# Kernel tuning notes

Measured on AMD Instinct MI355X. Metric: run time of the kernel, lower is better.

Reference implementation:

```python
import jax, jax.numpy as jnp
import numpy as np

B_SZ, SEQ, D_MODEL, D_STATE, DT_RANK = 2, 2048, 1024, 16, 64


def setup_inputs() -> dict:
    key = jax.random.key(0)
    ks = jax.random.split(key, 7)
    x = jax.random.normal(ks[0], (B_SZ, SEQ, D_MODEL), dtype=jnp.float32)
    dt_proj_input = jax.random.normal(ks[1], (B_SZ, SEQ, DT_RANK), dtype=jnp.float32)
    # A_log initialized as -log(arange(1, d_state+1)) per _initialize_parameters
    A_log = -jnp.log(jnp.arange(1, D_STATE + 1, dtype=jnp.float32))
    # dt_proj: weight ~ N(0, 0.1), bias = log(expm1(dt)) - 2 with dt ~ logU(dt_min, dt_max)
    dt_W = 0.1 * jax.random.normal(ks[2], (D_MODEL, DT_RANK), dtype=jnp.float32)
    u = jax.random.uniform(ks[3], (D_MODEL,), dtype=jnp.float32)
    dt = jnp.exp(u * (np.log(0.1) - np.log(0.001)) + np.log(0.001))
    dt = jnp.clip(dt, 0.0001, None)
    dt_b = jnp.log(jnp.expm1(dt)) - 2.0
    # B_proj / C_proj: xavier-uniform (d_state, d_model), no bias
    lim = np.sqrt(6.0 / (D_STATE + D_MODEL)).astype(np.float32)
    B_W = jax.random.uniform(ks[4], (D_STATE, D_MODEL), dtype=jnp.float32, minval=-lim, maxval=lim)
    C_W = jax.random.uniform(ks[5], (D_STATE, D_MODEL), dtype=jnp.float32, minval=-lim, maxval=lim)
    D_vec = jnp.ones((D_MODEL,), dtype=jnp.float32)
    return {"x": x, "dt_proj_input": dt_proj_input, "A_log": A_log,
            "dt_W": dt_W, "dt_b": dt_b, "B_W": B_W, "C_W": C_W, "D_vec": D_vec}


def reference(x, dt_proj_input, A_log, dt_W, dt_b, B_W, C_W, D_vec):
    # dt = softplus(Linear(dt_proj_input) + bias)  -- note bias is added twice, faithful to source
    dt = jax.nn.softplus(jnp.einsum('blr,dr->bld', dt_proj_input, dt_W) + 2.0 * dt_b)  # (b,l,d)
    Bm = jnp.einsum('bld,nd->bln', x, B_W)  # (b,l,n)
    Cm = jnp.einsum('bld,nd->bln', x, C_W)  # (b,l,n)
    A = -jnp.exp(A_log)                      # (n,)
    dA = jnp.exp(dt[..., None] * A)                                   # (b,l,d,n)
    dB = dt[..., None] * Bm[:, :, None, :] * x[..., None]             # (b,l,d,n)
    # linear recurrence h[t] = dA[t] * h[t-1] + dB[t]
    def step(h, ab):
        a, b = ab
        h = a * h + b
        return h, h
    h0 = jnp.zeros((x.shape[0], x.shape[2], A_log.shape[0]), dtype=x.dtype)
    _, states = jax.lax.scan(step, h0, (jnp.swapaxes(dA, 0, 1), jnp.swapaxes(dB, 0, 1)))
    states = jnp.swapaxes(states, 0, 1)      # (b,l,d,n)
    y = jnp.einsum('bldn,bln->bld', states, Cm)
    return y + x * D_vec
```

## Files before the change

kernel.cpp:

```cpp
#include <hip/hip_runtime.h>

#define LOG2E 1.44269504088896340736f
#define LN2   0.69314718055994530942f

constexpr int BSZ = 2, SEQ = 2048, DM = 1024, DS = 16, DR = 64;
constexpr int NC = 64, CL = SEQ / NC;

constexpr size_t OFF_DT   = 0;
constexpr size_t OFF_BM   = OFF_DT + (size_t)BSZ*SEQ*DM;
constexpr size_t OFF_CM   = OFF_BM + (size_t)BSZ*SEQ*DS;
constexpr size_t OFF_S    = OFF_CM + (size_t)BSZ*SEQ*DS;
constexpr size_t OFF_HEND = OFF_S  + (size_t)BSZ*NC*DM;
constexpr size_t OFF_HIN  = OFF_HEND + (size_t)BSZ*NC*DS*DM;
constexpr size_t OFF_PART = OFF_HIN  + (size_t)BSZ*NC*DS*DM;

__device__ inline float softplusf(float z) {
  float e = __builtin_amdgcn_exp2f(z * LOG2E);
  if (z > 15.f) return z;
  if (z < -8.f) return e;
  return __builtin_amdgcn_logf(1.f + e) * LN2;
}

__device__ inline void fma4(float& acc, float4 a, float4 b) {
  acc = fmaf(a.x, b.x, fmaf(a.y, b.y, fmaf(a.z, b.z, fmaf(a.w, b.w, acc))));
}

__global__ __launch_bounds__(256, 2) void k_front(const float* __restrict__ inp,
                                                  const float* __restrict__ W,
                                                  const float* __restrict__ bias,
                                                  float* __restrict__ dt,
                                                  const float* __restrict__ x,
                                                  const float* __restrict__ BW,
                                                  const float* __restrict__ CW,
                                                  float* __restrict__ part) {
  __shared__ __align__(16) float smem[16896];
  int bid = blockIdx.x;
  int t = threadIdx.x;
  if (bid < 256) {
    float* At = smem;
    float* Wt = smem + 64 * 132;
    int mt = bid >> 3, nt = bid & 7;
    int m0 = mt * 128, n0 = nt * 128;
#pragma unroll
    for (int i = 0; i < 8; ++i) {
      int idx4 = t + 256 * i;
      int m = idx4 >> 4, k4 = (idx4 & 15) * 4;
      float4 v = *(const float4*)&inp[(size_t)(m0 + m) * DR + k4];
      At[(k4 + 0) * 132 + m] = v.x; At[(k4 + 1) * 132 + m] = v.y;
      At[(k4 + 2) * 132 + m] = v.z; At[(k4 + 3) * 132 + m] = v.w;
    }
#pragma unroll
    for (int i = 0; i < 8; ++i) {
      int idx4 = t + 256 * i;
      int n = idx4 >> 4, k4 = (idx4 & 15) * 4;
      float4 v = *(const float4*)&W[(size_t)(n0 + n) * DR + k4];
      Wt[(k4 + 0) * 132 + n] = v.x; Wt[(k4 + 1) * 132 + n] = v.y;
      Wt[(k4 + 2) * 132 + n] = v.z; Wt[(k4 + 3) * 132 + n] = v.w;
    }
    __syncthreads();
    int mg = t >> 4, ng = t & 15;
    float acc[8][8] = {};
#pragma unroll 4
    for (int k = 0; k < 64; ++k) {
      const float* rowA = At + k * 132;
      const float* rowW = Wt + k * 132;
      float4 a0 = *(const float4*)&rowA[mg * 8];
      float4 a1 = *(const float4*)&rowA[mg * 8 + 4];
      float4 w0 = *(const float4*)&rowW[ng * 4];
      float4 w1 = *(const float4*)&rowW[ng * 4 + 64];
      float a[8] = {a0.x, a0.y, a0.z, a0.w, a1.x, a1.y, a1.z, a1.w};
      float w[8] = {w0.x, w0.y, w0.z, w0.w, w1.x, w1.y, w1.z, w1.w};
#pragma unroll
      for (int i = 0; i < 8; ++i)
#pragma unroll
        for (int j = 0; j < 8; ++j)
          acc[i][j] = fmaf(a[i], w[j], acc[i][j]);
    }
    float4 b0 = *(const float4*)&bias[n0 + ng * 4];
    float4 b1 = *(const float4*)&bias[n0 + ng * 4 + 64];
    float bb[8] = {b0.x, b0.y, b0.z, b0.w, b1.x, b1.y, b1.z, b1.w};
#pragma unroll
    for (int i = 0; i < 8; ++i) {
      int m = m0 + mg * 8 + i;
      float4 lo, hi;
      lo.x = softplusf(acc[i][0] + 2.f * bb[0]);
      lo.y = softplusf(acc[i][1] + 2.f * bb[1]);
      lo.z = softplusf(acc[i][2] + 2.f * bb[2]);
      lo.w = softplusf(acc[i][3] + 2.f * bb[3]);
      hi.x = softplusf(acc[i][4] + 2.f * bb[4]);
      hi.y = softplusf(acc[i][5] + 2.f * bb[5]);
      hi.z = softplusf(acc[i][6] + 2.f * bb[6]);
      hi.w = softplusf(acc[i][7] + 2.f * bb[7]);
      *(float4*)&dt[(size_t)m * DM + n0 + ng * 4]      = lo;
      *(float4*)&dt[(size_t)m * DM + n0 + ng * 4 + 64] = hi;
    }
  } else {
    float* xt = smem;
    float* wt = smem + 64 * 132;
    int bid2 = bid - 256;
    int mt = bid2 >> 3, ks = bid2 & 7;
    int m0 = mt * 64, k0 = ks * 128;
#pragma unroll
    for (int i = 0; i < 8; ++i) {
      int idx4 = t + 256 * i;
      int r = idx4 >> 5, c4 = (idx4 & 31) * 4;
      float4 v = *(const float4*)&x[(size_t)(m0 + r) * DM + k0 + c4];
      *(float4*)&xt[r * 132 + c4] = v;
    }
#pragma unroll
    for (int i = 0; i < 4; ++i) {
      int idx4 = t + 256 * i;
      int n = idx4 >> 5, c4 = (idx4 & 31) * 4;
      const float* src = (n < 16) ? &BW[(size_t)n * DM + k0 + c4]
                                  : &CW[(size_t)(n - 16) * DM + k0 + c4];
      *(float4*)&wt[n * 132 + c4] = *(const float4*)src;
    }
    __syncthreads();
    int lg = t >> 3, ng = t & 7;
    float acc[2][4] = {};
#pragma unroll 4
    for (int k4 = 0; k4 < 32; ++k4) {
      float4 xa0 = *(const float4*)&xt[(lg * 2 + 0) * 132 + k4 * 4];
      float4 xa1 = *(const float4*)&xt[(lg * 2 + 1) * 132 + k4 * 4];
#pragma unroll
      for (int j = 0; j < 4; ++j) {
        float4 w = *(const float4*)&wt[(ng + 8 * j) * 132 + k4 * 4];
        fma4(acc[0][j], xa0, w);
        fma4(acc[1][j], xa1, w);
      }
    }
#pragma unroll
    for (int i = 0; i < 2; ++i)
#pragma unroll
      for (int j = 0; j < 4; ++j)
        part[(size_t)ks * (4096 * 32) + (size_t)(m0 + lg * 2 + i) * 32 + ng + 8 * j] = acc[i][j];
  }
}

__global__ __launch_bounds__(256) void k_phase1(const float* __restrict__ x,
                                                const float* __restrict__ dt,
                                                const float* __restrict__ part,
                                                const float* __restrict__ A_log,
                                                float* __restrict__ Bm,
                                                float* __restrict__ Cm,
                                                float* __restrict__ Ssum,
                                                float* __restrict__ hend) {
  __shared__ float bml[CL * DS];
  int bid = blockIdx.x;
  int b = bid >> 8, rem = bid & 255;
  int c = rem >> 2, dg = rem & 3;
  int t = threadIdx.x;
  int d = dg * 256 + t;
  size_t blbase = (size_t)b * SEQ + c * CL;
  {
    size_t e = (blbase + (t >> 3)) * 32 + 2 * (t & 7);
    float2 s = make_float2(0.f, 0.f);
#pragma unroll
    for (int ks = 0; ks < 8; ++ks) {
      float2 v = *(const float2*)&part[(size_t)ks * (4096 * 32) + e];
      s.x += v.x; s.y += v.y;
    }
    *(float2*)&bml[t * 2] = s;
    if (dg == 0) {
      *(float2*)&Bm[(blbase + (t >> 3)) * DS + 2 * (t & 7)] = s;
      float2 sc = make_float2(0.f, 0.f);
#pragma unroll
      for (int ks = 0; ks < 8; ++ks) {
        float2 v = *(const float2*)&part[(size_t)ks * (4096 * 32) + e + 16];
        sc.x += v.x; sc.y += v.y;
      }
      *(float2*)&Cm[(blbase + (t >> 3)) * DS + 2 * (t & 7)] = sc;
    }
  }
  __syncthreads();
  float a2[16];
#pragma unroll
  for (int n = 0; n < 16; ++n)
    a2[n] = -__builtin_amdgcn_exp2f(A_log[n] * LOG2E) * LOG2E;
  float h[16] = {};
  float S = 0.f;
  size_t base = blbase * DM + d;
#pragma unroll 4
  for (int l = 0; l < CL; ++l) {
    float dtv = dt[base + (size_t)l * DM];
    float xv  = x[base + (size_t)l * DM];
    S += dtv;
    float dtx = dtv * xv;
#pragma unroll
    for (int n = 0; n < 16; ++n) {
      float a = __builtin_amdgcn_exp2f(dtv * a2[n]);
      h[n] = fmaf(a, h[n], dtx * bml[l * DS + n]);
    }
  }
  size_t cc = (size_t)b * NC + c;
  Ssum[cc * DM + d] = S;
#pragma unroll
  for (int n = 0; n < 16; ++n) hend[(cc * DS + n) * DM + d] = h[n];
}

__global__ __launch_bounds__(256) void k_phase2(const float* __restrict__ A_log,
                                                const float* __restrict__ Ssum,
                                                const float* __restrict__ hend,
                                                float* __restrict__ hin) {
  int bid = blockIdx.x;
  int b = bid >> 6, rem = bid & 63;
  int n = rem >> 2, dg = rem & 3;
  int d = dg * 256 + threadIdx.x;
  float a2 = -__builtin_amdgcn_exp2f(A_log[n] * LOG2E) * LOG2E;
  float h = 0.f;
#pragma unroll 8
  for (int c = 0; c < NC; ++c) {
    size_t cc = (size_t)b * NC + c;
    hin[(cc * DS + n) * DM + d] = h;
    float aa = __builtin_amdgcn_exp2f(a2 * Ssum[cc * DM + d]);
    h = fmaf(aa, h, hend[(cc * DS + n) * DM + d]);
  }
}

__global__ __launch_bounds__(256) void k_phase3(const float* __restrict__ x,
                                                const float* __restrict__ dt,
                                                const float* __restrict__ Bm,
                                                const float* __restrict__ Cm,
                                                const float* __restrict__ A_log,
                                                const float* __restrict__ Dvec,
                                                const float* __restrict__ hin,
                                                float* __restrict__ out) {
  __shared__ float bml[CL * DS], cml[CL * DS];
  int bid = blockIdx.x;
  int b = bid >> 8, rem = bid & 255;
  int c = rem >> 2, dg = rem & 3;
  int t = threadIdx.x;
  int d = dg * 256 + t;
  const float* bsrc = Bm + ((size_t)b * SEQ + c * CL) * DS;
  const float* csrc = Cm + ((size_t)b * SEQ + c * CL) * DS;
  *(float2*)&bml[t * 2] = *(const float2*)&bsrc[t * 2];
  *(float2*)&cml[t * 2] = *(const float2*)&csrc[t * 2];
  __syncthreads();
  float a2[16];
#pragma unroll
  for (int n = 0; n < 16; ++n)
    a2[n] = -__builtin_amdgcn_exp2f(A_log[n] * LOG2E) * LOG2E;
  size_t cc = (size_t)b * NC + c;
  float h[16];
#pragma unroll
  for (int n = 0; n < 16; ++n) h[n] = hin[(cc * DS + n) * DM + d];
  float dv = Dvec[d];
  size_t base = ((size_t)b * SEQ + c * CL) * DM + d;
#pragma unroll 4
  for (int l = 0; l < CL; ++l) {
    float dtv = dt[base + (size_t)l * DM];
    float xv  = x[base + (size_t)l * DM];
    float dtx = dtv * xv;
    float y = 0.f;
#pragma unroll
    for (int n = 0; n < 16; ++n) {
      float a = __builtin_amdgcn_exp2f(dtv * a2[n]);
      h[n] = fmaf(a, h[n], dtx * bml[l * DS + n]);
      y = fmaf(h[n], cml[l * DS + n], y);
    }
    out[base + (size_t)l * DM] = fmaf(xv, dv, y);
  }
}

extern "C" void kernel_launch(void* const* d_in, const int* in_sizes, int n_in,
                              void* d_out, int out_size, void* d_ws, size_t ws_size,
                              hipStream_t stream) {
  (void)in_sizes; (void)n_in; (void)out_size; (void)ws_size;
  const float* x     = (const float*)d_in[0];
  const float* dtp   = (const float*)d_in[1];
  const float* A_log = (const float*)d_in[2];
  const float* dtW   = (const float*)d_in[3];
  const float* dtb   = (const float*)d_in[4];
  const float* BW    = (const float*)d_in[5];
  const float* CW    = (const float*)d_in[6];
  const float* Dv    = (const float*)d_in[7];
  float* out = (float*)d_out;
  float* ws  = (float*)d_ws;

  float* dt   = ws + OFF_DT;
  float* Bm   = ws + OFF_BM;
  float* Cm   = ws + OFF_CM;
  float* S    = ws + OFF_S;
  float* hend = ws + OFF_HEND;
  float* hin  = ws + OFF_HIN;
  float* part = ws + OFF_PART;

  k_front <<<768, 256, 0, stream>>>(dtp, dtW, dtb, dt, x, BW, CW, part);
  k_phase1<<<512, 256, 0, stream>>>(x, dt, part, A_log, Bm, Cm, S, hend);
  k_phase2<<<128, 256, 0, stream>>>(A_log, S, hend, hin);
  k_phase3<<<512, 256, 0, stream>>>(x, dt, Bm, Cm, A_log, Dv, hin, out);
}
```

Before: 64.40 us.

## Split state dimension across lanes and halve K-split partials in front GEMM

The phase1 and phase3 scans now give each channel to two lanes, each handling 8 of the 16 state entries. In phase3 the two halves of y are combined with a cross-lane shuffle. Blocks shrink to 128 threads and the grid grows to 2048 blocks, which raises parallelism and cuts per-thread serial work and register use. The B/C projection in k_front now splits K four ways instead of eight, looping over two K tiles per block, so phase1 reduces fewer partials with float4 loads. In exchange, each lane loads dt and x twice and phase3 adds a shuffle per timestep.

New measurement: 72.14 us. +12.0%, slower.

```diff
diff --git a/kernel.cpp b/kernel.cpp
--- a/kernel.cpp
+++ b/kernel.cpp
@@ -7,10 +7,10 @@
 constexpr int NC = 64, CL = SEQ / NC;
 
 constexpr size_t OFF_DT   = 0;
-constexpr size_t OFF_BM   = OFF_DT + (size_t)BSZ*SEQ*DM;
-constexpr size_t OFF_CM   = OFF_BM + (size_t)BSZ*SEQ*DS;
-constexpr size_t OFF_S    = OFF_CM + (size_t)BSZ*SEQ*DS;
-constexpr size_t OFF_HEND = OFF_S  + (size_t)BSZ*NC*DM;
+constexpr size_t OFF_BM   = OFF_DT   + (size_t)BSZ*SEQ*DM;
+constexpr size_t OFF_CM   = OFF_BM   + (size_t)BSZ*SEQ*DS;
+constexpr size_t OFF_S    = OFF_CM   + (size_t)BSZ*SEQ*DS;
+constexpr size_t OFF_HEND = OFF_S    + (size_t)BSZ*NC*DM;
 constexpr size_t OFF_HIN  = OFF_HEND + (size_t)BSZ*NC*DS*DM;
 constexpr size_t OFF_PART = OFF_HIN  + (size_t)BSZ*NC*DS*DM;
 
@@ -98,35 +98,39 @@
     float* xt = smem;
     float* wt = smem + 64 * 132;
     int bid2 = bid - 256;
-    int mt = bid2 >> 3, ks = bid2 & 7;
-    int m0 = mt * 64, k0 = ks * 128;
-#pragma unroll
-    for (int i = 0; i < 8; ++i) {
-      int idx4 = t + 256 * i;
-      int r = idx4 >> 5, c4 = (idx4 & 31) * 4;
-      float4 v = *(const float4*)&x[(size_t)(m0 + r) * DM + k0 + c4];
-      *(float4*)&xt[r * 132 + c4] = v;
-    }
-#pragma unroll
-    for (int i = 0; i < 4; ++i) {
-      int idx4 = t + 256 * i;
-      int n = idx4 >> 5, c4 = (idx4 & 31) * 4;
-      const float* src = (n < 16) ? &BW[(size_t)n * DM + k0 + c4]
-                                  : &CW[(size_t)(n - 16) * DM + k0 + c4];
-      *(float4*)&wt[n * 132 + c4] = *(const float4*)src;
-    }
-    __syncthreads();
+    int mt = bid2 >> 2, ks = bid2 & 3;
+    int m0 = mt * 64, k0 = ks * 256;
     int lg = t >> 3, ng = t & 7;
     float acc[2][4] = {};
+#pragma unroll
+    for (int kh = 0; kh < 2; ++kh) {
+      int kb = k0 + kh * 128;
+      __syncthreads();
+#pragma unroll
+      for (int i = 0; i < 8; ++i) {
+        int idx4 = t + 256 * i;
+        int r = idx4 >> 5, c4 = (idx4 & 31) * 4;
+        *(float4*)&xt[r * 132 + c4] = *(const float4*)&x[(size_t)(m0 + r) * DM + kb + c4];
+      }
+#pragma unroll
+      for (int i = 0; i < 4; ++i) {
+        int idx4 = t + 256 * i;
+        int n = idx4 >> 5, c4 = (idx4 & 31) * 4;
+        const float* src = (n < 16) ? &BW[(size_t)n * DM + kb + c4]
+                                    : &CW[(size_t)(n - 16) * DM + kb + c4];
+        *(float4*)&wt[n * 132 + c4] = *(const float4*)src;
+      }
+      __syncthreads();
 #pragma unroll 4
-    for (int k4 = 0; k4 < 32; ++k4) {
-      float4 xa0 = *(const float4*)&xt[(lg * 2 + 0) * 132 + k4 * 4];
-      float4 xa1 = *(const float4*)&xt[(lg * 2 + 1) * 132 + k4 * 4];
-#pragma unroll
-      for (int j = 0; j < 4; ++j) {
-        float4 w = *(const float4*)&wt[(ng + 8 * j) * 132 + k4 * 4];
-        fma4(acc[0][j], xa0, w);
-        fma4(acc[1][j], xa1, w);
+      for (int k4 = 0; k4 < 32; ++k4) {
+        float4 xa0 = *(const float4*)&xt[(lg * 2 + 0) * 132 + k4 * 4];
+        float4 xa1 = *(const float4*)&xt[(lg * 2 + 1) * 132 + k4 * 4];
+#pragma unroll
+        for (int j = 0; j < 4; ++j) {
+          float4 w = *(const float4*)&wt[(ng + 8 * j) * 132 + k4 * 4];
+          fma4(acc[0][j], xa0, w);
+          fma4(acc[1][j], xa1, w);
+        }
       }
     }
 #pragma unroll
@@ -137,47 +141,45 @@
   }
 }
 
-__global__ __launch_bounds__(256) void k_phase1(const float* __restrict__ x,
-                                                const float* __restrict__ dt,
-                                                const float* __restrict__ part,
-                                                const float* __restrict__ A_log,
-                                                float* __restrict__ Bm,
-                                                float* __restrict__ Cm,
-                                                float* __restrict__ Ssum,
-                                                float* __restrict__ hend) {
+__global__ __launch_bounds__(128, 4) void k_phase1(const float* __restrict__ x,
+                                                   const float* __restrict__ dt,
+                                                   const float* __restrict__ part,
+                                                   const float* __restrict__ A_log,
+                                                   float* __restrict__ Bm,
+                                                   float* __restrict__ Cm,
+                                                   float* __restrict__ Ssum,
+                                                   float* __restrict__ hend) {
   __shared__ float bml[CL * DS];
   int bid = blockIdx.x;
-  int b = bid >> 8, rem = bid & 255;
-  int c = rem >> 2, dg = rem & 3;
+  int b = bid >> 10, c = (bid >> 4) & 63, dg = bid & 15;
   int t = threadIdx.x;
-  int d = dg * 256 + t;
+  int lane = t & 63, w = t >> 6;
+  int nh = lane >> 5;
+  int d = dg * 64 + (lane & 31) + w * 32;
   size_t blbase = (size_t)b * SEQ + c * CL;
   {
-    size_t e = (blbase + (t >> 3)) * 32 + 2 * (t & 7);
-    float2 s = make_float2(0.f, 0.f);
-#pragma unroll
-    for (int ks = 0; ks < 8; ++ks) {
-      float2 v = *(const float2*)&part[(size_t)ks * (4096 * 32) + e];
-      s.x += v.x; s.y += v.y;
-    }
-    *(float2*)&bml[t * 2] = s;
+    int l = t >> 2, q = (t & 3) * 4;
+    size_t e = (blbase + l) * 32 + q;
+    float4 sb = make_float4(0.f, 0.f, 0.f, 0.f), sc = sb;
+#pragma unroll
+    for (int ks = 0; ks < 4; ++ks) {
+      float4 vb = *(const float4*)&part[(size_t)ks * (4096 * 32) + e];
+      float4 vc = *(const float4*)&part[(size_t)ks * (4096 * 32) + e + 16];
+      sb.x += vb.x; sb.y += vb.y; sb.z += vb.z; sb.w += vb.w;
+      sc.x += vc.x; sc.y += vc.y; sc.z += vc.z; sc.w += vc.w;
+    }
+    *(float4*)&bml[t * 4] = sb;
     if (dg == 0) {
-      *(float2*)&Bm[(blbase + (t >> 3)) * DS + 2 * (t & 7)] = s;
-      float2 sc = make_float2(0.f, 0.f);
-#pragma unroll
-      for (int ks = 0; ks < 8; ++ks) {
-        float2 v = *(const float2*)&part[(size_t)ks * (4096 * 32) + e + 16];
-        sc.x += v.x; sc.y += v.y;
-      }
-      *(float2*)&Cm[(blbase + (t >> 3)) * DS + 2 * (t & 7)] = sc;
+      *(float4*)&Bm[(blbase + l) * DS + q] = sb;
+      *(float4*)&Cm[(blbase + l) * DS + q] = sc;
     }
   }
   __syncthreads();
-  float a2[16];
-#pragma unroll
-  for (int n = 0; n < 16; ++n)
-    a2[n] = -__builtin_amdgcn_exp2f(A_log[n] * LOG2E) * LOG2E;
-  float h[16] = {};
+  float a2[8];
+#pragma unroll
+  for (int j = 0; j < 8; ++j)
+    a2[j] = -__builtin_amdgcn_exp2f(A_log[nh * 8 + j] * LOG2E) * LOG2E;
+  float h[8] = {};
   float S = 0.f;
   size_t base = blbase * DM + d;
 #pragma unroll 4
@@ -186,79 +188,89 @@
     float xv  = x[base + (size_t)l * DM];
     S += dtv;
     float dtx = dtv * xv;
-#pragma unroll
-    for (int n = 0; n < 16; ++n) {
-      float a = __builtin_amdgcn_exp2f(dtv * a2[n]);
-      h[n] = fmaf(a, h[n], dtx * bml[l * DS + n]);
+    const float* bq = &bml[l * DS + nh * 8];
+#pragma unroll
+    for (int j = 0; j < 8; ++j) {
+      float a = __builtin_amdgcn_exp2f(dtv * a2[j]);
+      h[j] = fmaf(a, h[j], dtx * bq[j]);
     }
   }
   size_t cc = (size_t)b * NC + c;
-  Ssum[cc * DM + d] = S;
-#pragma unroll
-  for (int n = 0; n < 16; ++n) hend[(cc * DS + n) * DM + d] = h[n];
-}
-
-__global__ __launch_bounds__(256) void k_phase2(const float* __restrict__ A_log,
-                                                const float* __restrict__ Ssum,
-                                                const float* __restrict__ hend,
-                                                float* __restrict__ hin) {
+  if (nh == 0) Ssum[cc * DM + d] = S;
+#pragma unroll
+  for (int j = 0; j < 8; ++j) hend[(cc * DS + nh * 8 + j) * DM + d] = h[j];
+}
+
+__global__ __launch_bounds__(128, 4) void k_phase2(const float* __restrict__ A_log,
+                                                   const float* __restrict__ Ssum,
+                                                   const float* __restrict__ hend,
+                                                   float* __restrict__ hin) {
   int bid = blockIdx.x;
-  int b = bid >> 6, rem = bid & 63;
-  int n = rem >> 2, dg = rem & 3;
-  int d = dg * 256 + threadIdx.x;
-  float a2 = -__builtin_amdgcn_exp2f(A_log[n] * LOG2E) * LOG2E;
+  int b = bid >> 7, n = (bid >> 3) & 15, dg = bid & 7;
+  int d = dg * 128 + threadIdx.x;
+  float a2n = -__builtin_amdgcn_exp2f(A_log[n] * LOG2E) * LOG2E;
   float h = 0.f;
 #pragma unroll 8
   for (int c = 0; c < NC; ++c) {
     size_t cc = (size_t)b * NC + c;
     hin[(cc * DS + n) * DM + d] = h;
-    float aa = __builtin_amdgcn_exp2f(a2 * Ssum[cc * DM + d]);
+    float aa = __builtin_amdgcn_exp2f(a2n * Ssum[cc * DM + d]);
     h = fmaf(aa, h, hend[(cc * DS + n) * DM + d]);
   }
 }
 
-__global__ __launch_bounds__(256) void k_phase3(const float* __restrict__ x,
-                                                const float* __restrict__ dt,
-                                                const float* __restrict__ Bm,
-                                                const float* __restrict__ Cm,
-                                                const float* __restrict__ A_log,
-                                                const float* __restrict__ Dvec,
-                                                const float* __restrict__ hin,
-                                                float* __restrict__ out) {
+__global__ __launch_bounds__(128, 4) void k_phase3(const float* __restrict__ x,
+                                                   const float* __restrict__ dt,
+                                                   const float* __restrict__ Bm,
+                                                   const float* __restrict__ Cm,
+                                                   const float* __restrict__ A_log,
+                                                   const float* __restrict__ Dvec,
+                                                   const float* __restrict__ hin,
+                                                   float* __restrict__ out) {
   __shared__ float bml[CL * DS], cml[CL * DS];
   int bid = blockIdx.x;
-  int b = bid >> 8, rem = bid & 255;
-  int c = rem >> 2, dg = rem & 3;
+  int b = bid >> 10, c = (bid >> 4) & 63, dg = bid & 15;
   int t = threadIdx.x;
-  int d = dg * 256 + t;
-  const float* bsrc = Bm + ((size_t)b * SEQ + c * CL) * DS;
-  const float* csrc = Cm + ((size_t)b * SEQ + c * CL) * DS;
-  *(float2*)&bml[t * 2] = *(const float2*)&bsrc[t * 2];
-  *(float2*)&cml[t * 2] = *(const float2*)&csrc[t * 2];
+  int lane = t & 63, w = t >> 6;
+  int nh = lane >> 5;
+  int d = dg * 64 + (lane & 31) + w * 32;
+  size_t blbase = (size_t)b * SEQ + c * CL;
+  *(float4*)&bml[t * 4] = *(const float4*)&Bm[blbase * DS + t * 4];
+  *(float4*)&cml[t * 4] = *(const float4*)&Cm[blbase * DS + t * 4];
   __syncthreads();
-  float a2[16];
-#pragma unroll
-  for (int n = 0; n < 16; ++n)
-    a2[n] = -__builtin_amdgcn_exp2f(A_log[n] * LOG2E) * LOG2E;
+  float a2[8];
+#pragma unroll
+  for (int j = 0; j < 8; ++j)
+    a2[j] = -__builtin_amdgcn_exp2f(A_log[nh * 8 + j] * LOG2E) * LOG2E;
   size_t cc = (size_t)b * NC + c;
-  float h[16];
-#pragma unroll
-  for (int n = 0; n < 16; ++n) h[n] = hin[(cc * DS + n) * DM + d];
-  float dv = Dvec[d];
-  size_t base = ((size_t)b * SEQ + c * CL) * DM + d;
+  float h[8];
+#pragma unroll
+  for (int j = 0; j < 8; ++j) h[j] = hin[(cc * DS + nh * 8 + j) * DM + d];
+  float dvl = (nh == 0) ? Dvec[d] : 0.f;
+  size_t base = blbase * DM + d;
 #pragma unroll 4
   for (int l = 0; l < CL; ++l) {
     float dtv = dt[base + (size_t)l * DM];
     float xv  = x[base + (size_t)l * DM];
     float dtx = dtv * xv;
-    float y = 0.f;
-#pragma unroll
-    for (int n = 0; n < 16; ++n) {
-      float a = __builtin_amdgcn_exp2f(dtv * a2[n]);
-      h[n] = fmaf(a, h[n], dtx * bml[l * DS + n]);
-      y = fmaf(h[n], cml[l * DS + n], y);
-    }
-    out[base + (size_t)l * DM] = fmaf(xv, dv, y);
+    const float* bq = &bml[l * DS + nh * 8];
+    const float* cq = &cml[l * DS + nh * 8];
+    float y0 = xv * dvl, y1 = 0.f;
+#pragma unroll
+    for (int j = 0; j < 4; ++j) {
+      float a = __builtin_amdgcn_exp2f(dtv * a2[j]);
+      h[j] = fmaf(a, h[j], dtx * bq[j]);
+      y0 = fmaf(h[j], cq[j], y0);
+    }
+#pragma unroll
+    for (int j = 4; j < 8; ++j) {
+      float a = __builtin_amdgcn_exp2f(dtv * a2[j]);
+      h[j] = fmaf(a, h[j], dtx * bq[j]);
+      y1 = fmaf(h[j], cq[j], y1);
+    }
+    float y = y0 + y1;
+    y += __shfl_xor(y, 32);
+    if (nh == 0) out[base + (size_t)l * DM] = y;
   }
 }
 
@@ -285,8 +297,8 @@
   float* hin  = ws + OFF_HIN;
   float* part = ws + OFF_PART;
 
-  k_front <<<768, 256, 0, stream>>>(dtp, dtW, dtb, dt, x, BW, CW, part);
-  k_phase1<<<512, 256, 0, stream>>>(x, dt, part, A_log, Bm, Cm, S, hend);
-  k_phase2<<<128, 256, 0, stream>>>(A_log, S, hend, hin);
-  k_phase3<<<512, 256, 0, stream>>>(x, dt, Bm, Cm, A_log, Dv, hin, out);
-}
+  k_front <<<512,  256, 0, stream>>>(dtp, dtW, dtb, dt, x, BW, CW, part);
+  k_phase1<<<2048, 128, 0, stream>>>(x, dt, part, A_log, Bm, Cm, S, hend);
+  k_phase2<<<256,  128, 0, stream>>>(A_log, S, hend, hin);
+  k_phase3<<<2048, 128, 0, stream>>>(x, dt, Bm, Cm, A_log, Dv, hin, out);
+}
```

## Fuse chunked scan phases into one cooperative kernel with grid syncs

Applied to the files above, without the earlier changes.

Replaces the three scan kernels with a single cooperative kernel over 1024 blocks and 128 shorter chunks. Each thread keeps its local outputs and cumulative dt in registers, the inter-chunk carry runs between two grid syncs, and the result is corrected with the carried-in state, so dt and x are not re-read in a third pass. The front kernel's B/C projection now splits K four ways instead of eight, halving the partial sums to reduce. The fused path depends on cooperative launch and an occupancy of at least 4 blocks per CU, otherwise it falls back to the old kernels. Large register arrays and a serial carry loop on only 512 blocks of 64 threads risk spills and idle time.

After: 64.76 us. About the same (+0.6%).

```diff
diff --git a/kernel.cpp b/kernel.cpp
--- a/kernel.cpp
+++ b/kernel.cpp
@@ -1,18 +1,22 @@
 #include <hip/hip_runtime.h>
+#include <hip/hip_cooperative_groups.h>
+
+namespace cg = cooperative_groups;
 
 #define LOG2E 1.44269504088896340736f
 #define LN2   0.69314718055994530942f
 
 constexpr int BSZ = 2, SEQ = 2048, DM = 1024, DS = 16, DR = 64;
 constexpr int NC = 64, CL = SEQ / NC;
+constexpr int NCF = 128, CLF = SEQ / NCF;
 
 constexpr size_t OFF_DT   = 0;
-constexpr size_t OFF_BM   = OFF_DT + (size_t)BSZ*SEQ*DM;
-constexpr size_t OFF_CM   = OFF_BM + (size_t)BSZ*SEQ*DS;
-constexpr size_t OFF_S    = OFF_CM + (size_t)BSZ*SEQ*DS;
-constexpr size_t OFF_HEND = OFF_S  + (size_t)BSZ*NC*DM;
-constexpr size_t OFF_HIN  = OFF_HEND + (size_t)BSZ*NC*DS*DM;
-constexpr size_t OFF_PART = OFF_HIN  + (size_t)BSZ*NC*DS*DM;
+constexpr size_t OFF_BM   = OFF_DT   + (size_t)BSZ*SEQ*DM;
+constexpr size_t OFF_CM   = OFF_BM   + (size_t)BSZ*SEQ*DS;
+constexpr size_t OFF_S    = OFF_CM   + (size_t)BSZ*SEQ*DS;
+constexpr size_t OFF_HEND = OFF_S    + (size_t)BSZ*NCF*DM;
+constexpr size_t OFF_HIN  = OFF_HEND + (size_t)BSZ*NCF*DS*DM;
+constexpr size_t OFF_PART = OFF_HIN  + (size_t)BSZ*NCF*DS*DM;
 
 __device__ inline float softplusf(float z) {
   float e = __builtin_amdgcn_exp2f(z * LOG2E);
@@ -98,35 +102,39 @@
     float* xt = smem;
     float* wt = smem + 64 * 132;
     int bid2 = bid - 256;
-    int mt = bid2 >> 3, ks = bid2 & 7;
-    int m0 = mt * 64, k0 = ks * 128;
-#pragma unroll
-    for (int i = 0; i < 8; ++i) {
-      int idx4 = t + 256 * i;
-      int r = idx4 >> 5, c4 = (idx4 & 31) * 4;
-      float4 v = *(const float4*)&x[(size_t)(m0 + r) * DM + k0 + c4];
-      *(float4*)&xt[r * 132 + c4] = v;
-    }
-#pragma unroll
-    for (int i = 0; i < 4; ++i) {
-      int idx4 = t + 256 * i;
-      int n = idx4 >> 5, c4 = (idx4 & 31) * 4;
-      const float* src = (n < 16) ? &BW[(size_t)n * DM + k0 + c4]
-                                  : &CW[(size_t)(n - 16) * DM + k0 + c4];
-      *(float4*)&wt[n * 132 + c4] = *(const float4*)src;
-    }
-    __syncthreads();
+    int mt = bid2 >> 2, ks = bid2 & 3;
+    int m0 = mt * 64, k0 = ks * 256;
     int lg = t >> 3, ng = t & 7;
     float acc[2][4] = {};
+#pragma unroll
+    for (int kh = 0; kh < 2; ++kh) {
+      int kb = k0 + kh * 128;
+      __syncthreads();
+#pragma unroll
+      for (int i = 0; i < 8; ++i) {
+        int idx4 = t + 256 * i;
+        int r = idx4 >> 5, c4 = (idx4 & 31) * 4;
+        *(float4*)&xt[r * 132 + c4] = *(const float4*)&x[(size_t)(m0 + r) * DM + kb + c4];
+      }
+#pragma unroll
+      for (int i = 0; i < 4; ++i) {
+        int idx4 = t + 256 * i;
+        int n = idx4 >> 5, c4 = (idx4 & 31) * 4;
+        const float* src = (n < 16) ? &BW[(size_t)n * DM + kb + c4]
+                                    : &CW[(size_t)(n - 16) * DM + kb + c4];
+        *(float4*)&wt[n * 132 + c4] = *(const float4*)src;
+      }
+      __syncthreads();
 #pragma unroll 4
-    for (int k4 = 0; k4 < 32; ++k4) {
-      float4 xa0 = *(const float4*)&xt[(lg * 2 + 0) * 132 + k4 * 4];
-      float4 xa1 = *(const float4*)&xt[(lg * 2 + 1) * 132 + k4 * 4];
-#pragma unroll
-      for (int j = 0; j < 4; ++j) {
-        float4 w = *(const float4*)&wt[(ng + 8 * j) * 132 + k4 * 4];
-        fma4(acc[0][j], xa0, w);
-        fma4(acc[1][j], xa1, w);
+      for (int k4 = 0; k4 < 32; ++k4) {
+        float4 xa0 = *(const float4*)&xt[(lg * 2 + 0) * 132 + k4 * 4];
+        float4 xa1 = *(const float4*)&xt[(lg * 2 + 1) * 132 + k4 * 4];
+#pragma unroll
+        for (int j = 0; j < 4; ++j) {
+          float4 w = *(const float4*)&wt[(ng + 8 * j) * 132 + k4 * 4];
+          fma4(acc[0][j], xa0, w);
+          fma4(acc[1][j], xa1, w);
+        }
       }
     }
 #pragma unroll
@@ -134,6 +142,106 @@
 #pragma unroll
       for (int j = 0; j < 4; ++j)
         part[(size_t)ks * (4096 * 32) + (size_t)(m0 + lg * 2 + i) * 32 + ng + 8 * j] = acc[i][j];
+  }
+}
+
+__global__ __launch_bounds__(256, 4) void k_scan_fused(const float* __restrict__ x,
+                                                       const float* __restrict__ dtg,
+                                                       const float* __restrict__ part,
+                                                       const float* __restrict__ A_log,
+                                                       const float* __restrict__ Dv,
+                                                       float* __restrict__ Ssum,
+                                                       float* __restrict__ hend,
+                                                       float* __restrict__ hin,
+                                                       float* __restrict__ out) {
+  cg::grid_group grid = cg::this_grid();
+  __shared__ float bml[CLF * DS], cml[CLF * DS];
+  int bid = blockIdx.x, t = threadIdx.x;
+  int b = bid >> 9, c = (bid >> 2) & 127, dg = bid & 3;
+  int d = dg * 256 + t;
+  size_t blbase = (size_t)b * SEQ + (size_t)c * CLF;
+  size_t cc = (size_t)b * NCF + c;
+
+  {
+    int idx = t & 127, l = idx >> 3, pr = idx & 7;
+    int col = pr * 2 + ((t >= 128) ? 16 : 0);
+    size_t e = (blbase + l) * 32 + col;
+    float2 s = make_float2(0.f, 0.f);
+#pragma unroll
+    for (int ks = 0; ks < 4; ++ks) {
+      float2 v = *(const float2*)&part[(size_t)ks * (4096 * 32) + e];
+      s.x += v.x; s.y += v.y;
+    }
+    float* dst = (t < 128) ? bml : cml;
+    *(float2*)&dst[l * DS + pr * 2] = s;
+  }
+  __syncthreads();
+  float a2[16];
+#pragma unroll
+  for (int n = 0; n < 16; ++n)
+    a2[n] = -__builtin_amdgcn_exp2f(A_log[n] * LOG2E) * LOG2E;
+  float Tl[CLF], yl[CLF], h[16] = {};
+  float dv = Dv[d];
+  float T = 0.f;
+  size_t base = blbase * DM + d;
+#pragma unroll
+  for (int l = 0; l < CLF; ++l) {
+    float dtv = dtg[base + (size_t)l * DM];
+    float xv  = x[base + (size_t)l * DM];
+    T += dtv; Tl[l] = T;
+    float dtx = dtv * xv;
+    float y = xv * dv;
+    float bq[16], cq[16];
+#pragma unroll
+    for (int u = 0; u < 4; ++u) {
+      *(float4*)&bq[4 * u] = *(const float4*)&bml[l * DS + 4 * u];
+      *(float4*)&cq[4 * u] = *(const float4*)&cml[l * DS + 4 * u];
+    }
+#pragma unroll
+    for (int n = 0; n < 16; ++n) {
+      float a = __builtin_amdgcn_exp2f(dtv * a2[n]);
+      h[n] = fmaf(a, h[n], dtx * bq[n]);
+      y = fmaf(h[n], cq[n], y);
+    }
+    yl[l] = y;
+  }
+  Ssum[cc * DM + d] = T;
+#pragma unroll
+  for (int n = 0; n < 16; ++n) hend[(cc * DS + n) * DM + d] = h[n];
+
+  grid.sync();
+
+  if (bid < 512 && t < 64) {
+    int b2 = bid >> 8, n = (bid >> 4) & 15, ds16 = bid & 15;
+    int d2 = ds16 * 64 + t;
+    float a2n = -__builtin_amdgcn_exp2f(A_log[n] * LOG2E) * LOG2E;
+    float hh = 0.f;
+#pragma unroll 8
+    for (int c2 = 0; c2 < NCF; ++c2) {
+      size_t cc2 = (size_t)b2 * NCF + c2;
+      hin[(cc2 * DS + n) * DM + d2] = hh;
+      float aa = __builtin_amdgcn_exp2f(a2n * Ssum[cc2 * DM + d2]);
+      hh = fmaf(aa, hh, hend[(cc2 * DS + n) * DM + d2]);
+    }
+  }
+
+  grid.sync();
+
+  float hn[16];
+#pragma unroll
+  for (int n = 0; n < 16; ++n) hn[n] = hin[(cc * DS + n) * DM + d];
+#pragma unroll
+  for (int l = 0; l < CLF; ++l) {
+    float y = yl[l];
+#pragma unroll
+    for (int u = 0; u < 4; ++u) {
+      float4 cq = *(const float4*)&cml[l * DS + 4 * u];
+      y = fmaf(cq.x * hn[4 * u + 0], __builtin_amdgcn_exp2f(a2[4 * u + 0] * Tl[l]), y);
+      y = fmaf(cq.y * hn[4 * u + 1], __builtin_amdgcn_exp2f(a2[4 * u + 1] * Tl[l]), y);
+      y = fmaf(cq.z * hn[4 * u + 2], __builtin_amdgcn_exp2f(a2[4 * u + 2] * Tl[l]), y);
+      y = fmaf(cq.w * hn[4 * u + 3], __builtin_amdgcn_exp2f(a2[4 * u + 3] * Tl[l]), y);
+    }
+    out[base + (size_t)l * DM] = y;
   }
 }
 
@@ -147,28 +255,22 @@
                                                 float* __restrict__ hend) {
   __shared__ float bml[CL * DS];
   int bid = blockIdx.x;
-  int b = bid >> 8, rem = bid & 255;
-  int c = rem >> 2, dg = rem & 3;
+  int b = bid >> 8, c = (bid >> 2) & 63, dg = bid & 3;
   int t = threadIdx.x;
   int d = dg * 256 + t;
   size_t blbase = (size_t)b * SEQ + c * CL;
   {
     size_t e = (blbase + (t >> 3)) * 32 + 2 * (t & 7);
-    float2 s = make_float2(0.f, 0.f);
-#pragma unroll
-    for (int ks = 0; ks < 8; ++ks) {
-      float2 v = *(const float2*)&part[(size_t)ks * (4096 * 32) + e];
-      s.x += v.x; s.y += v.y;
-    }
-    *(float2*)&bml[t * 2] = s;
+    float2 sb = make_float2(0.f, 0.f), sc = make_float2(0.f, 0.f);
+#pragma unroll
+    for (int ks = 0; ks < 4; ++ks) {
+      float2 vb = *(const float2*)&part[(size_t)ks * (4096 * 32) + e];
+      float2 vc = *(const float2*)&part[(size_t)ks * (4096 * 32) + e + 16];
+      sb.x += vb.x; sb.y += vb.y; sc.x += vc.x; sc.y += vc.y;
+    }
+    *(float2*)&bml[t * 2] = sb;
     if (dg == 0) {
-      *(float2*)&Bm[(blbase + (t >> 3)) * DS + 2 * (t & 7)] = s;
-      float2 sc = make_float2(0.f, 0.f);
-#pragma unroll
-      for (int ks = 0; ks < 8; ++ks) {
-        float2 v = *(const float2*)&part[(size_t)ks * (4096 * 32) + e + 16];
-        sc.x += v.x; sc.y += v.y;
-      }
+      *(float2*)&Bm[(blbase + (t >> 3)) * DS + 2 * (t & 7)] = sb;
       *(float2*)&Cm[(blbase + (t >> 3)) * DS + 2 * (t & 7)] = sc;
     }
   }
@@ -203,16 +305,15 @@
                                                 const float* __restrict__ hend,
                                                 float* __restrict__ hin) {
   int bid = blockIdx.x;
-  int b = bid >> 6, rem = bid & 63;
-  int n = rem >> 2, dg = rem & 3;
+  int b = bid >> 6, n = (bid >> 2) & 15, dg = bid & 3;
   int d = dg * 256 + threadIdx.x;
-  float a2 = -__builtin_amdgcn_exp2f(A_log[n] * LOG2E) * LOG2E;
+  float a2n = -__builtin_amdgcn_exp2f(A_log[n] * LOG2E) * LOG2E;
   float h = 0.f;
 #pragma unroll 8
   for (int c = 0; c < NC; ++c) {
     size_t cc = (size_t)b * NC + c;
     hin[(cc * DS + n) * DM + d] = h;
-    float aa = __builtin_amdgcn_exp2f(a2 * Ssum[cc * DM + d]);
+    float aa = __builtin_amdgcn_exp2f(a2n * Ssum[cc * DM + d]);
     h = fmaf(aa, h, hend[(cc * DS + n) * DM + d]);
   }
 }
@@ -227,8 +328,7 @@
                                                 float* __restrict__ out) {
   __shared__ float bml[CL * DS], cml[CL * DS];
   int bid = blockIdx.x;
-  int b = bid >> 8, rem = bid & 255;
-  int c = rem >> 2, dg = rem & 3;
+  int b = bid >> 8, c = (bid >> 2) & 63, dg = bid & 3;
   int t = threadIdx.x;
   int d = dg * 256 + t;
   const float* bsrc = Bm + ((size_t)b * SEQ + c * CL) * DS;
@@ -285,7 +385,21 @@
   float* hin  = ws + OFF_HIN;
   float* part = ws + OFF_PART;
 
-  k_front <<<768, 256, 0, stream>>>(dtp, dtW, dtb, dt, x, BW, CW, part);
+  k_front<<<512, 256, 0, stream>>>(dtp, dtW, dtb, dt, x, BW, CW, part);
+
+  int nb = 0;
+  hipError_t oe = hipOccupancyMaxActiveBlocksPerMultiprocessor(&nb, k_scan_fused, 256, 0);
+  bool coop_ok = (oe == hipSuccess && nb >= 4);
+  if (coop_ok) {
+    const float* xx = x; const float* dd = dt; const float* pp = part;
+    const float* al = A_log; const float* dv = Dv;
+    float* ss = S; float* he = hend; float* hi = hin; float* oo = out;
+    void* kargs[] = {(void*)&xx, (void*)&dd, (void*)&pp, (void*)&al, (void*)&dv,
+                     (void*)&ss, (void*)&he, (void*)&hi, (void*)&oo};
+    hipError_t le = hipLaunchCooperativeKernel((const void*)k_scan_fused,
+                                               dim3(1024), dim3(256), kargs, 0, stream);
+    if (le == hipSuccess) return;
+  }
   k_phase1<<<512, 256, 0, stream>>>(x, dt, part, A_log, Bm, Cm, S, hend);
   k_phase2<<<128, 256, 0, stream>>>(A_log, S, hend, hin);
   k_phase3<<<512, 256, 0, stream>>>(x, dt, Bm, Cm, A_log, Dv, hin, out);
```

## Double scan chunk count, parallelize inter-chunk pass, halve split-K partials

Applied to the files above, without the earlier changes.

Doubles the number of sequence chunks to 128, so the phase-1 and phase-3 scan kernels launch twice as many blocks with half the sequential length each. The inter-chunk carry kernel now splits the 128 chunks into four segments per thread group, computes local prefix states and cumulative dt sums, and combines the segments through shared memory, giving more blocks and shorter serial chains. The B/C projection in the front kernel now uses split-K of 4 with two K-halves per block, which halves the partial-sum traffic read in phase 1. In exchange, the workspace traffic for hend and hin doubles and phase 2 holds 64 extra registers per thread.

Result: slower. 70.72 us (+9.8%).

```diff
diff --git a/kernel.cpp b/kernel.cpp
--- a/kernel.cpp
+++ b/kernel.cpp
@@ -4,13 +4,13 @@
 #define LN2   0.69314718055994530942f
 
 constexpr int BSZ = 2, SEQ = 2048, DM = 1024, DS = 16, DR = 64;
-constexpr int NC = 64, CL = SEQ / NC;
+constexpr int NC = 128, CL = SEQ / NC;
 
 constexpr size_t OFF_DT   = 0;
-constexpr size_t OFF_BM   = OFF_DT + (size_t)BSZ*SEQ*DM;
-constexpr size_t OFF_CM   = OFF_BM + (size_t)BSZ*SEQ*DS;
-constexpr size_t OFF_S    = OFF_CM + (size_t)BSZ*SEQ*DS;
-constexpr size_t OFF_HEND = OFF_S  + (size_t)BSZ*NC*DM;
+constexpr size_t OFF_BM   = OFF_DT   + (size_t)BSZ*SEQ*DM;
+constexpr size_t OFF_CM   = OFF_BM   + (size_t)BSZ*SEQ*DS;
+constexpr size_t OFF_S    = OFF_CM   + (size_t)BSZ*SEQ*DS;
+constexpr size_t OFF_HEND = OFF_S    + (size_t)BSZ*NC*DM;
 constexpr size_t OFF_HIN  = OFF_HEND + (size_t)BSZ*NC*DS*DM;
 constexpr size_t OFF_PART = OFF_HIN  + (size_t)BSZ*NC*DS*DM;
 
@@ -98,35 +98,39 @@
     float* xt = smem;
     float* wt = smem + 64 * 132;
     int bid2 = bid - 256;
-    int mt = bid2 >> 3, ks = bid2 & 7;
-    int m0 = mt * 64, k0 = ks * 128;
-#pragma unroll
-    for (int i = 0; i < 8; ++i) {
-      int idx4 = t + 256 * i;
-      int r = idx4 >> 5, c4 = (idx4 & 31) * 4;
-      float4 v = *(const float4*)&x[(size_t)(m0 + r) * DM + k0 + c4];
-      *(float4*)&xt[r * 132 + c4] = v;
-    }
-#pragma unroll
-    for (int i = 0; i < 4; ++i) {
-      int idx4 = t + 256 * i;
-      int n = idx4 >> 5, c4 = (idx4 & 31) * 4;
-      const float* src = (n < 16) ? &BW[(size_t)n * DM + k0 + c4]
-                                  : &CW[(size_t)(n - 16) * DM + k0 + c4];
-      *(float4*)&wt[n * 132 + c4] = *(const float4*)src;
-    }
-    __syncthreads();
+    int mt = bid2 >> 2, ks = bid2 & 3;
+    int m0 = mt * 64, k0 = ks * 256;
     int lg = t >> 3, ng = t & 7;
     float acc[2][4] = {};
+#pragma unroll
+    for (int kh = 0; kh < 2; ++kh) {
+      int kb = k0 + kh * 128;
+      __syncthreads();
+#pragma unroll
+      for (int i = 0; i < 8; ++i) {
+        int idx4 = t + 256 * i;
+        int r = idx4 >> 5, c4 = (idx4 & 31) * 4;
+        *(float4*)&xt[r * 132 + c4] = *(const float4*)&x[(size_t)(m0 + r) * DM + kb + c4];
+      }
+#pragma unroll
+      for (int i = 0; i < 4; ++i) {
+        int idx4 = t + 256 * i;
+        int n = idx4 >> 5, c4 = (idx4 & 31) * 4;
+        const float* src = (n < 16) ? &BW[(size_t)n * DM + kb + c4]
+                                    : &CW[(size_t)(n - 16) * DM + kb + c4];
+        *(float4*)&wt[n * 132 + c4] = *(const float4*)src;
+      }
+      __syncthreads();
 #pragma unroll 4
-    for (int k4 = 0; k4 < 32; ++k4) {
-      float4 xa0 = *(const float4*)&xt[(lg * 2 + 0) * 132 + k4 * 4];
-      float4 xa1 = *(const float4*)&xt[(lg * 2 + 1) * 132 + k4 * 4];
-#pragma unroll
-      for (int j = 0; j < 4; ++j) {
-        float4 w = *(const float4*)&wt[(ng + 8 * j) * 132 + k4 * 4];
-        fma4(acc[0][j], xa0, w);
-        fma4(acc[1][j], xa1, w);
+      for (int k4 = 0; k4 < 32; ++k4) {
+        float4 xa0 = *(const float4*)&xt[(lg * 2 + 0) * 132 + k4 * 4];
+        float4 xa1 = *(const float4*)&xt[(lg * 2 + 1) * 132 + k4 * 4];
+#pragma unroll
+        for (int j = 0; j < 4; ++j) {
+          float4 w = *(const float4*)&wt[(ng + 8 * j) * 132 + k4 * 4];
+          fma4(acc[0][j], xa0, w);
+          fma4(acc[1][j], xa1, w);
+        }
       }
     }
 #pragma unroll
@@ -147,29 +151,24 @@
                                                 float* __restrict__ hend) {
   __shared__ float bml[CL * DS];
   int bid = blockIdx.x;
-  int b = bid >> 8, rem = bid & 255;
-  int c = rem >> 2, dg = rem & 3;
+  int b = bid >> 9, c = (bid >> 2) & 127, dg = bid & 3;
   int t = threadIdx.x;
   int d = dg * 256 + t;
-  size_t blbase = (size_t)b * SEQ + c * CL;
+  size_t blbase = (size_t)b * SEQ + (size_t)c * CL;
   {
-    size_t e = (blbase + (t >> 3)) * 32 + 2 * (t & 7);
+    int idx = t & 127, l = idx >> 3, pr = idx & 7;
+    int col = pr * 2 + ((t >= 128) ? 16 : 0);
+    size_t e = (blbase + l) * 32 + col;
     float2 s = make_float2(0.f, 0.f);
 #pragma unroll
-    for (int ks = 0; ks < 8; ++ks) {
+    for (int ks = 0; ks < 4; ++ks) {
       float2 v = *(const float2*)&part[(size_t)ks * (4096 * 32) + e];
       s.x += v.x; s.y += v.y;
     }
-    *(float2*)&bml[t * 2] = s;
+    if (t < 128) *(float2*)&bml[l * DS + pr * 2] = s;
     if (dg == 0) {
-      *(float2*)&Bm[(blbase + (t >> 3)) * DS + 2 * (t & 7)] = s;
-      float2 sc = make_float2(0.f, 0.f);
-#pragma unroll
-      for (int ks = 0; ks < 8; ++ks) {
-        float2 v = *(const float2*)&part[(size_t)ks * (4096 * 32) + e + 16];
-        sc.x += v.x; sc.y += v.y;
-      }
-      *(float2*)&Cm[(blbase + (t >> 3)) * DS + 2 * (t & 7)] = sc;
+      float* dstg = (t < 128) ? Bm : Cm;
+      *(float2*)&dstg[(blbase + l) * DS + pr * 2] = s;
     }
   }
   __syncthreads();
@@ -202,18 +201,35 @@
                                                 const float* __restrict__ Ssum,
                                                 const float* __restrict__ hend,
                                                 float* __restrict__ hin) {
+  __shared__ float Eq[4][64], Tq[4][64];
   int bid = blockIdx.x;
-  int b = bid >> 6, rem = bid & 63;
-  int n = rem >> 2, dg = rem & 3;
-  int d = dg * 256 + threadIdx.x;
-  float a2 = -__builtin_amdgcn_exp2f(A_log[n] * LOG2E) * LOG2E;
-  float h = 0.f;
-#pragma unroll 8
-  for (int c = 0; c < NC; ++c) {
+  int b = bid >> 8, n = (bid >> 4) & 15, dgrp = bid & 15;
+  int t = threadIdx.x;
+  int q = t >> 6, lane = t & 63;
+  int d = dgrp * 64 + lane;
+  float a2n = -__builtin_amdgcn_exp2f(A_log[n] * LOG2E) * LOG2E;
+  float Tpre[32], hlp[32];
+  float H = 0.f, T = 0.f;
+#pragma unroll
+  for (int j = 0; j < 32; ++j) {
+    int c = q * 32 + j;
     size_t cc = (size_t)b * NC + c;
-    hin[(cc * DS + n) * DM + d] = h;
-    float aa = __builtin_amdgcn_exp2f(a2 * Ssum[cc * DM + d]);
-    h = fmaf(aa, h, hend[(cc * DS + n) * DM + d]);
+    Tpre[j] = T; hlp[j] = H;
+    float s = Ssum[cc * DM + d];
+    float e = hend[(cc * DS + n) * DM + d];
+    H = fmaf(__builtin_amdgcn_exp2f(a2n * s), H, e);
+    T += s;
+  }
+  Eq[q][lane] = H; Tq[q][lane] = T;
+  __syncthreads();
+  float Hin = 0.f;
+  for (int p = 0; p < q; ++p)
+    Hin = fmaf(__builtin_amdgcn_exp2f(a2n * Tq[p][lane]), Hin, Eq[p][lane]);
+#pragma unroll
+  for (int j = 0; j < 32; ++j) {
+    int c = q * 32 + j;
+    size_t cc = (size_t)b * NC + c;
+    hin[(cc * DS + n) * DM + d] = fmaf(__builtin_amdgcn_exp2f(a2n * Tpre[j]), Hin, hlp[j]);
   }
 }
 
@@ -227,14 +243,12 @@
                                                 float* __restrict__ out) {
   __shared__ float bml[CL * DS], cml[CL * DS];
   int bid = blockIdx.x;
-  int b = bid >> 8, rem = bid & 255;
-  int c = rem >> 2, dg = rem & 3;
+  int b = bid >> 9, c = (bid >> 2) & 127, dg = bid & 3;
   int t = threadIdx.x;
   int d = dg * 256 + t;
-  const float* bsrc = Bm + ((size_t)b * SEQ + c * CL) * DS;
-  const float* csrc = Cm + ((size_t)b * SEQ + c * CL) * DS;
-  *(float2*)&bml[t * 2] = *(const float2*)&bsrc[t * 2];
-  *(float2*)&cml[t * 2] = *(const float2*)&csrc[t * 2];
+  size_t blbase = (size_t)b * SEQ + (size_t)c * CL;
+  if (t < 64)       *(float4*)&bml[t * 4]        = *(const float4*)&Bm[blbase * DS + t * 4];
+  else if (t < 128) *(float4*)&cml[(t - 64) * 4] = *(const float4*)&Cm[blbase * DS + (t - 64) * 4];
   __syncthreads();
   float a2[16];
 #pragma unroll
@@ -245,7 +259,7 @@
 #pragma unroll
   for (int n = 0; n < 16; ++n) h[n] = hin[(cc * DS + n) * DM + d];
   float dv = Dvec[d];
-  size_t base = ((size_t)b * SEQ + c * CL) * DM + d;
+  size_t base = blbase * DM + d;
 #pragma unroll 4
   for (int l = 0; l < CL; ++l) {
     float dtv = dt[base + (size_t)l * DM];
@@ -285,8 +299,8 @@
   float* hin  = ws + OFF_HIN;
   float* part = ws + OFF_PART;
 
-  k_front <<<768, 256, 0, stream>>>(dtp, dtW, dtb, dt, x, BW, CW, part);
-  k_phase1<<<512, 256, 0, stream>>>(x, dt, part, A_log, Bm, Cm, S, hend);
-  k_phase2<<<128, 256, 0, stream>>>(A_log, S, hend, hin);
-  k_phase3<<<512, 256, 0, stream>>>(x, dt, Bm, Cm, A_log, Dv, hin, out);
-}
+  k_front <<<512,  256, 0, stream>>>(dtp, dtW, dtb, dt, x, BW, CW, part);
+  k_phase1<<<1024, 256, 0, stream>>>(x, dt, part, A_log, Bm, Cm, S, hend);
+  k_phase2<<<512,  256, 0, stream>>>(A_log, S, hend, hin);
+  k_phase3<<<1024, 256, 0, stream>>>(x, dt, Bm, Cm, A_log, Dv, hin, out);
+}
```
